# Performance work log

Hardware: AMD Instinct MI355X
Metric: run time of the kernel (lower is better)

Reference implementation:

```python
import jax, jax.numpy as jnp
import numpy as np

B, S, H, W, T, D = 256, 128, 14, 14, 12, 512


def _lin(key, fan_in, fan_out):
    k1, k2 = jax.random.split(key)
    bound = 1.0 / np.sqrt(fan_in)
    Wm = jax.random.uniform(k1, (fan_in, fan_out), jnp.float32, -bound, bound)
    b = jax.random.uniform(k2, (fan_out,), jnp.float32, -bound, bound)
    return Wm, b


def setup_inputs() -> dict:
    key = jax.random.key(0)
    ks = jax.random.split(key, 20)
    inp = {
        "ci_1": jax.random.normal(ks[0], (B, D), jnp.float32),
        "mi_1": jax.random.normal(ks[1], (B, D), jnp.float32),
        "q": jax.random.normal(ks[2], (B, D), jnp.float32),
        "cws": jax.random.normal(ks[3], (B, S, D), jnp.float32),
        "K": jax.random.normal(ks[4], (B, H, W, D), jnp.float32),
        "C_past": jax.random.normal(ks[5], (B, T, D), jnp.float32),
        "M_past": jax.random.normal(ks[6], (B, T, D), jnp.float32),
    }
    inp["W_cq"], inp["b_cq"] = _lin(ks[7], D, D)          # control_qi
    inp["W_cqi"], inp["b_cqi"] = _lin(ks[8], 2 * D, D)    # cqi_linear
    inp["W_cai"], inp["b_cai"] = _lin(ks[9], D, 1)        # cais_linear
    inp["W_rm"], inp["b_rm"] = _lin(ks[10], D, D)         # memory_read_m
    inp["W_rk"], inp["b_rk"] = _lin(ks[11], D, D)         # memory_read_k
    inp["W_rik"], inp["b_rik"] = _lin(ks[12], 2 * D, D)   # memory_read_ik
    inp["W_rci"], inp["b_rci"] = _lin(ks[13], D, D)       # memory_read_ci_i
    inp["W_wrm"], inp["b_wrm"] = _lin(ks[14], 2 * D, D)   # memory_write_ri_mi_1
    inp["W_wcc"], inp["b_wcc"] = _lin(ks[15], D, 1)       # memory_write_ci_cj
    inp["W_wsa"], inp["b_wsa"] = _lin(ks[16], D, D)       # memory_write_mi_sa
    inp["W_winfo"], inp["b_winfo"] = _lin(ks[17], D, D)   # memory_write_mi_info
    inp["W_wci"], inp["b_wci"] = _lin(ks[18], D, 1)       # memory_write_ci
    return inp


def reference(ci_1, mi_1, q, cws, K, C_past, M_past,
              W_cq, b_cq, W_cqi, b_cqi, W_cai, b_cai,
              W_rm, b_rm, W_rk, b_rk, W_rik, b_rik, W_rci, b_rci,
              W_wrm, b_wrm, W_wcc, b_wcc, W_wsa, b_wsa,
              W_winfo, b_winfo, W_wci, b_wci):
    # ---- control ----
    qi = q @ W_cq + b_cq                                        # [B,D]
    cqi = jnp.concatenate([ci_1, qi], axis=1) @ W_cqi + b_cqi   # [B,D]
    cqi_cws = cqi[:, None, :] * cws                             # [B,S,D]
    cai = cqi_cws @ W_cai + b_cai                               # [B,S,1]
    cvis = jax.nn.softmax(cai, axis=1)
    ci = (cvis * cws).sum(axis=1)                               # [B,D]

    # ---- read ----
    Ii = (mi_1 @ W_rm + b_rm)[:, None, None, :] * (K @ W_rk + b_rk)  # [B,H,W,D]
    Ii_prime = jnp.concatenate([Ii, K], axis=3) @ W_rik + b_rik      # [B,H,W,D]
    rai = (ci[:, None, None, :] * Ii_prime) @ W_rci + b_rci          # [B,H,W,D]
    rvi = jax.nn.softmax(rai, axis=1)   # softmax over H
    rvi = jax.nn.softmax(rvi, axis=2)   # then softmax of those probs over W (faithful)
    ri = (rvi * K).sum(axis=(1, 2))                                  # [B,D]

    # ---- write ----
    mi_info = jnp.concatenate([ri, mi_1], axis=1) @ W_wrm + b_wrm    # [B,D]
    ci_cj = ci[:, None, :] * C_past                                  # [B,T,D]
    saij = jax.nn.softmax(ci_cj @ W_wcc + b_wcc, axis=1)             # [B,T,1]
    mi_sa = (saij * M_past).sum(axis=1)                              # [B,D]
    mi_prime = (mi_sa @ W_wsa + b_wsa) + (mi_info @ W_winfo + b_winfo)
    gate = jax.nn.sigmoid(ci @ W_wci + b_wci)                        # [B,1]
    mi = gate * mi_1 + (1.0 - gate) * mi_prime
    return (ci, mi)
```

## Files before the change

kernel.cpp:

```cpp
#include <hip/hip_runtime.h>
#include <hip/hip_bf16.h>

typedef unsigned short u16;
typedef __attribute__((ext_vector_type(8))) short short8;
typedef __attribute__((ext_vector_type(4))) float f4;

static __device__ __forceinline__ float b2f(u16 u) {
    union { unsigned int i; float f; } x; x.i = ((unsigned int)u) << 16; return x.f;
}
static __device__ __forceinline__ u16 f2b(float f) {
    union { float f; unsigned int i; } x; x.f = f;
    unsigned int r = x.i + 0x7fffu + ((x.i >> 16) & 1u);
    return (u16)(r >> 16);
}
static __device__ __forceinline__ float wave_reduce_sum(float v) {
    #pragma unroll
    for (int off = 32; off > 0; off >>= 1) v += __shfl_down(v, off, 64);
    return v;
}
static __device__ __forceinline__ void gl2lds(const void* g, void* l) {
    __builtin_amdgcn_global_load_lds(
        (const __attribute__((address_space(1))) void*)g,
        (__attribute__((address_space(3))) void*)l, 16, 0, 0);
}

__global__ __launch_bounds__(256) void conv_f32_bf16(
    const float* __restrict__ src, u16* __restrict__ dst, int n)
{
    int i = (blockIdx.x * 256 + threadIdx.x) * 4;
    if (i >= n) return;
    float4 v = *(const float4*)(src + i);
    union { u16 u[4]; uint2 d; } o;
    o.u[0] = f2b(v.x); o.u[1] = f2b(v.y); o.u[2] = f2b(v.z); o.u[3] = f2b(v.w);
    *(uint2*)(dst + i) = o.d;
}

__global__ __launch_bounds__(256) void transpose_k(
    const float* __restrict__ in, u16* __restrict__ out,
    int K, int N, int out_stride, int k_off)
{
    __shared__ float t[32][33];
    int kb = blockIdx.x * 32, nb = blockIdx.y * 32;
    int tx = threadIdx.x, ty = threadIdx.y;
    #pragma unroll
    for (int i = 0; i < 4; i++)
        t[ty + i * 8][tx] = in[(size_t)(kb + ty + i * 8) * N + nb + tx];
    __syncthreads();
    #pragma unroll
    for (int i = 0; i < 4; i++)
        out[(size_t)(nb + ty + i * 8) * out_stride + k_off + kb + tx] =
            f2b(t[tx][ty + i * 8]);
}

template<int MT, int NT>
__global__ __launch_bounds__(256) void gemm_mfma(
    const u16* __restrict__ A0, const u16* __restrict__ A1,
    int M, int K0, int K1, int N,
    const u16* __restrict__ Bt,
    const float* __restrict__ bias0, const float* __restrict__ bias1,
    int epi_mode, const float* __restrict__ E, int m_div,
    const float* __restrict__ gate, const float* __restrict__ mi1,
    void* __restrict__ Cout, int out_f32)
{
    constexpr int BM = MT * 32, BN = NT * 32;
    constexpr int STG = (BM + BN) * 32;
    constexpr int NPF = MT / 2 + NT / 2;
    constexpr int STAGE_B = 3 * STG * 2;
    __shared__ __align__(16) char smem[STAGE_B];
    short* stg = (short*)smem;

    int tid  = threadIdx.x;
    int wave = tid >> 6, lane = tid & 63;
    int wm = wave >> 1, wn = wave & 1;
    int lrow = lane & 15, quad = lane >> 4;

    int gx = gridDim.x, gy = gridDim.y;
    int bx = blockIdx.x, by = blockIdx.y;
    if ((gy & 7) == 0) {
        int lin = by * gx + bx;
        int xcd = lin & 7, j = lin >> 3;
        by = xcd * (gy >> 3) + j / gx;
        bx = j % gx;
    }
    int bm0 = by * BM, bn0 = bx * BN;
    int Ktot = K0 + K1;
    int KT = Ktot >> 5;

    int r16 = lane >> 2, cc = lane & 3;
    int sw = (r16 >> 1) & 3;
    int coff = (cc ^ sw) * 8;

    auto stage = [&](int s, int k0) {
        const u16* asrc; int lda;
        if (k0 < K0) { asrc = A0 + k0; lda = K0; }
        else         { asrc = A1 + (k0 - K0); lda = K1; }
        short* As = stg + s * STG;
        short* Bs = As + BM * 32;
        #pragma unroll
        for (int i = 0; i < MT / 2; i++) {
            int ar = wave * (BM / 4) + 16 * i;
            gl2lds(asrc + (size_t)(bm0 + ar + r16) * lda + coff, As + ar * 32);
        }
        #pragma unroll
        for (int i = 0; i < NT / 2; i++) {
            int br = wave * (BN / 4) + 16 * i;
            gl2lds(Bt + (size_t)(bn0 + br + r16) * Ktot + k0 + coff, Bs + br * 32);
        }
    };

    f4 acc[MT][NT];
    #pragma unroll
    for (int i = 0; i < MT; i++)
        #pragma unroll
        for (int j = 0; j < NT; j++)
            acc[i][j] = (f4){0.f, 0.f, 0.f, 0.f};

    stage(0, 0);
    if (KT > 1) stage(1, 32);
    int sb = 0;
    int sw2 = (lrow >> 1) & 3;
    for (int kt = 0; kt < KT; kt++) {
        if (kt + 1 < KT) {
            if constexpr (NPF == 2)
                asm volatile("s_waitcnt vmcnt(2) lgkmcnt(0)\ns_barrier" ::: "memory");
            else
                asm volatile("s_waitcnt vmcnt(0) lgkmcnt(0)\ns_barrier" ::: "memory");
        } else {
            asm volatile("s_waitcnt vmcnt(0) lgkmcnt(0)\ns_barrier" ::: "memory");
        }
        const short* Ab = stg + sb * STG;
        const short* Bb = Ab + BM * 32;
        if (kt + 2 < KT) {
            int s2 = sb + 2; if (s2 >= 3) s2 -= 3;
            stage(s2, (kt + 2) * 32);
        }
        short8 af[MT], bfr[NT];
        #pragma unroll
        for (int mt = 0; mt < MT; mt++)
            af[mt] = *(const short8*)&Ab[(wm * (MT * 16) + mt * 16 + lrow) * 32 + (quad ^ sw2) * 8];
        #pragma unroll
        for (int nt = 0; nt < NT; nt++)
            bfr[nt] = *(const short8*)&Bb[(wn * (NT * 16) + nt * 16 + lrow) * 32 + (quad ^ sw2) * 8];
        #pragma unroll
        for (int mt = 0; mt < MT; mt++)
            #pragma unroll
            for (int nt = 0; nt < NT; nt++)
                acc[mt][nt] = __builtin_amdgcn_mfma_f32_16x16x32_bf16(
                    af[mt], bfr[nt], acc[mt][nt], 0, 0, 0);
        sb = (sb + 1 == 3) ? 0 : sb + 1;
    }

    #pragma unroll
    for (int nt = 0; nt < NT; nt++) {
        int n = bn0 + wn * (NT * 16) + nt * 16 + lrow;
        float bv = 0.f;
        if (bias0) bv += bias0[n];
        if (bias1) bv += bias1[n];
        #pragma unroll
        for (int mt = 0; mt < MT; mt++) {
            #pragma unroll
            for (int r = 0; r < 4; r++) {
                int m = bm0 + wm * (MT * 16) + mt * 16 + quad * 4 + r;
                float v = acc[mt][nt][r] + bv;
                if (epi_mode == 1) {
                    v *= E[(size_t)(m / m_div) * N + n];
                } else if (epi_mode == 2) {
                    float g = gate[m];
                    v = g * mi1[(size_t)m * N + n] + (1.f - g) * v;
                }
                if (out_f32) ((float*)Cout)[(size_t)m * N + n] = v;
                else         ((u16*)Cout)[(size_t)m * N + n] = f2b(v);
            }
        }
    }
}

__global__ __launch_bounds__(512, 2) void fused_read(
    const u16* __restrict__ kbf, int M,
    const u16* __restrict__ Wrk,  const float* __restrict__ brk,  const float* __restrict__ E1,
    const u16* __restrict__ Wrik, const float* __restrict__ brik, const float* __restrict__ E2,
    const u16* __restrict__ Wrci, const float* __restrict__ brci,
    u16* __restrict__ rai)
{
    __shared__ __align__(16) char smem[139264];
    short* g_tile = (short*)smem;
    short* stgbase = (short*)(smem + 65536);

    int tid = threadIdx.x, wave = tid >> 6, lane = tid & 63;
    int wr = wave >> 2, wc = wave & 3;
    int lrow = lane & 15, quad = lane >> 4;
    int r16 = lane >> 2, cc = lane & 3;
    int sw = (r16 >> 1) & 3;
    int coff = (cc ^ sw) * 8;
    int sw2 = (lrow >> 1) & 3;

    int bid = blockIdx.x;
    { int nb = gridDim.x; if ((nb & 7) == 0) { int x = bid & 7, j = bid >> 3; bid = x * (nb >> 3) + j; } }
    int bm0 = bid * 64;

    auto stageB = [&](short* bf, const u16* Wt, int ldk, int k0) {
        short* Bs = bf + 2048;
        #pragma unroll
        for (int i = 0; i < 4; i++) {
            int br = wave * 64 + i * 16;
            gl2lds(Wt + (size_t)(br + r16) * ldk + k0 + coff, Bs + br * 32);
        }
    };
    auto stageA = [&](short* bf, int k0) {
        if (wave < 4) {
            int ar = wave * 16;
            gl2lds(kbf + (size_t)(bm0 + ar + r16) * 512 + k0 + coff, bf + ar * 32);
        }
    };

    f4 acc[2][8];
    auto clr = [&]() {
        #pragma unroll
        for (int t = 0; t < 2; t++)
            #pragma unroll
            for (int nt = 0; nt < 8; nt++)
                acc[t][nt] = (f4){0.f, 0.f, 0.f, 0.f};
    };

    auto kstep = [&](const short* bf, int aMode, int kc0) {
        short8 af[2], bfrag[8];
        #pragma unroll
        for (int t = 0; t < 2; t++) {
            int R = wr * 32 + t * 16 + lrow;
            if (aMode == 0)
                af[t] = *(const short8*)&bf[R * 32 + (quad ^ sw2) * 8];
            else {
                int kc = kc0 + quad;
                af[t] = *(const short8*)&g_tile[R * 512 + ((kc ^ (R & 7)) << 3)];
            }
        }
        const short* Bs = bf + 2048;
        #pragma unroll
        for (int nt = 0; nt < 8; nt++)
            bfrag[nt] = *(const short8*)&Bs[(wc * 128 + nt * 16 + lrow) * 32 + (quad ^ sw2) * 8];
        #pragma unroll
        for (int t = 0; t < 2; t++)
            #pragma unroll
            for (int nt = 0; nt < 8; nt++)
                acc[t][nt] = __builtin_amdgcn_mfma_f32_16x16x32_bf16(
                    af[t], bfrag[nt], acc[t][nt], 0, 0, 0);
    };

    int b0 = bm0 / 196, b1 = (bm0 + 63) / 196;
    int rsw = (b1 != b0) ? (b1 * 196 - bm0) : 64;
    auto epi_to_gtile = [&](const float* bias, const float* E) {
        #pragma unroll
        for (int nt = 0; nt < 8; nt++) {
            int n = wc * 128 + nt * 16 + lrow;
            float bv = bias[n];
            float e0 = E[(size_t)b0 * 512 + n];
            float e1 = E[(size_t)b1 * 512 + n];
            #pragma unroll
            for (int t = 0; t < 2; t++)
                #pragma unroll
                for (int r = 0; r < 4; r++) {
                    int row = wr * 32 + t * 16 + quad * 4 + r;
                    float e = (row < rsw) ? e0 : e1;
                    u16 h = f2b((acc[t][nt][r] + bv) * e);
                    int chunk = (n >> 3) ^ (row & 7);
                    g_tile[row * 512 + chunk * 8 + (n & 7)] = (short)h;
                }
        }
    };

    clr();
    stageA(stgbase, 0); stageB(stgbase, Wrk, 512, 0);
    for (int kt = 0; kt < 16; kt++) {
        short* cur = stgbase + (kt & 1) * 18432;
        short* nxt = stgbase + ((kt & 1) ^ 1) * 18432;
        if (kt + 1 < 16) {
            stageA(nxt, (kt + 1) * 32); stageB(nxt, Wrk, 512, (kt + 1) * 32);
            if (wave < 4) asm volatile("s_waitcnt vmcnt(5) lgkmcnt(0)\ns_barrier" ::: "memory");
            else          asm volatile("s_waitcnt vmcnt(4) lgkmcnt(0)\ns_barrier" ::: "memory");
        } else
            asm volatile("s_waitcnt vmcnt(0) lgkmcnt(0)\ns_barrier" ::: "memory");
        kstep(cur, 0, 0);
        __syncthreads();
    }
    epi_to_gtile(brk, E1);
    __syncthreads();

    clr();
    stageB(stgbase, Wrik, 1024, 0);
    for (int kt = 0; kt < 16; kt++) {
        short* cur = stgbase + (kt & 1) * 18432;
        short* nxt = stgbase + ((kt & 1) ^ 1) * 18432;
        if (kt + 1 < 16) {
            stageB(nxt, Wrik, 1024, (kt + 1) * 32);
            asm volatile("s_waitcnt vmcnt(4) lgkmcnt(0)\ns_barrier" ::: "memory");
        } else
            asm volatile("s_waitcnt vmcnt(0) lgkmcnt(0)\ns_barrier" ::: "memory");
        kstep(cur, 1, kt * 4);
        __syncthreads();
    }
    stageA(stgbase, 0); stageB(stgbase, Wrik, 1024, 512);
    for (int kt = 0; kt < 16; kt++) {
        short* cur = stgbase + (kt & 1) * 18432;
        short* nxt = stgbase + ((kt & 1) ^ 1) * 18432;
        if (kt + 1 < 16) {
            stageA(nxt, (kt + 1) * 32); stageB(nxt, Wrik, 1024, 512 + (kt + 1) * 32);
            if (wave < 4) asm volatile("s_waitcnt vmcnt(5) lgkmcnt(0)\ns_barrier" ::: "memory");
            else          asm volatile("s_waitcnt vmcnt(4) lgkmcnt(0)\ns_barrier" ::: "memory");
        } else
            asm volatile("s_waitcnt vmcnt(0) lgkmcnt(0)\ns_barrier" ::: "memory");
        kstep(cur, 0, 0);
        __syncthreads();
    }
    epi_to_gtile(brik, E2);
    __syncthreads();

    clr();
    stageB(stgbase, Wrci, 512, 0);
    for (int kt = 0; kt < 16; kt++) {
        short* cur = stgbase + (kt & 1) * 18432;
        short* nxt = stgbase + ((kt & 1) ^ 1) * 18432;
        if (kt + 1 < 16) {
            stageB(nxt, Wrci, 512, (kt + 1) * 32);
            asm volatile("s_waitcnt vmcnt(4) lgkmcnt(0)\ns_barrier" ::: "memory");
        } else
            asm volatile("s_waitcnt vmcnt(0) lgkmcnt(0)\ns_barrier" ::: "memory");
        kstep(cur, 1, kt * 4);
        __syncthreads();
    }
    #pragma unroll
    for (int nt = 0; nt < 8; nt++) {
        int n = wc * 128 + nt * 16 + lrow;
        float bv = brci[n];
        #pragma unroll
        for (int t = 0; t < 2; t++)
            #pragma unroll
            for (int r = 0; r < 4; r++) {
                int row = wr * 32 + t * 16 + quad * 4 + r;
                g_tile[row * 512 + n] = (short)f2b(acc[t][nt][r] + bv);
            }
    }
    __syncthreads();
    #pragma unroll
    for (int p = 0; p < 8; p++) {
        int idx = p * 512 + tid;
        short8 v = *(const short8*)&g_tile[idx * 8];
        *(short8*)&rai[(size_t)bm0 * 512 + (size_t)idx * 8] = v;
    }
}

__global__ __launch_bounds__(256) void control_attn(
    const float* __restrict__ cqi, const float* __restrict__ cws,
    const float* __restrict__ Wcai, const float* __restrict__ bcai,
    float* __restrict__ ci_f32, float* __restrict__ ci_out)
{
    int b = blockIdx.x, tid = threadIdx.x;
    __shared__ float tW[512];
    __shared__ float p[128];
    __shared__ float inv_l;
    for (int d = tid; d < 512; d += 256)
        tW[d] = cqi[(size_t)b * 512 + d] * Wcai[d];
    __syncthreads();
    int wave = tid >> 6, lane = tid & 63;
    const float* cwsb = cws + (size_t)b * 128 * 512;
    for (int s = wave; s < 128; s += 4) {
        const float* row = cwsb + (size_t)s * 512 + lane * 8;
        float acc = 0.f;
        #pragma unroll
        for (int j = 0; j < 8; j++) acc += tW[lane * 8 + j] * row[j];
        acc = wave_reduce_sum(acc);
        if (lane == 0) p[s] = acc + bcai[0];
    }
    __syncthreads();
    if (tid == 0) {
        float m = -1e30f;
        for (int s = 0; s < 128; s++) m = fmaxf(m, p[s]);
        float l = 0.f;
        for (int s = 0; s < 128; s++) { float e = __expf(p[s] - m); p[s] = e; l += e; }
        inv_l = 1.f / l;
    }
    __syncthreads();
    float inv = inv_l;
    for (int d = tid; d < 512; d += 256) {
        float acc = 0.f;
        for (int s = 0; s < 128; s++) acc += p[s] * cwsb[(size_t)s * 512 + d];
        acc *= inv;
        ci_f32[(size_t)b * 512 + d] = acc;
        ci_out[(size_t)b * 512 + d] = acc;
    }
}

__global__ __launch_bounds__(256) void read_reduce(
    const u16* __restrict__ rai, const u16* __restrict__ Kb, u16* __restrict__ ri)
{
    int b = blockIdx.x >> 1;
    int d = ((blockIdx.x & 1) << 8) + threadIdx.x;
    const u16* rb = rai + (size_t)b * 196 * 512 + d;
    const u16* kb = Kb + (size_t)b * 196 * 512 + d;
    float m1[14], il1[14];
    #pragma unroll
    for (int w = 0; w < 14; w++) {
        float m = -1e30f, s = 0.f;
        #pragma unroll
        for (int h = 0; h < 14; h++) {
            float v = b2f(rb[(size_t)(h * 14 + w) * 512]);
            float nm = fmaxf(m, v);
            s = s * __expf(m - nm) + __expf(v - nm);
            m = nm;
        }
        m1[w] = m; il1[w] = 1.f / s;
    }
    float acc = 0.f;
    #pragma unroll
    for (int h = 0; h < 14; h++) {
        float pv[14], ss = 0.f;
        #pragma unroll
        for (int w = 0; w < 14; w++) {
            float pr = __expf(b2f(rb[(size_t)(h * 14 + w) * 512]) - m1[w]) * il1[w];
            float e = __expf(pr);
            pv[w] = e; ss += e;
        }
        float il2 = 1.f / ss;
        #pragma unroll
        for (int w = 0; w < 14; w++)
            acc += pv[w] * il2 * b2f(kb[(size_t)(h * 14 + w) * 512]);
    }
    ri[(size_t)b * 512 + d] = f2b(acc);
}

__global__ __launch_bounds__(256) void write_attn(
    const float* __restrict__ ci_f32, const float* __restrict__ C_past,
    const float* __restrict__ M_past,
    const float* __restrict__ Wwcc, const float* __restrict__ bwcc,
    const float* __restrict__ Wwci, const float* __restrict__ bwci,
    u16* __restrict__ mi_sa, float* __restrict__ gate)
{
    int b = blockIdx.x, tid = threadIdx.x;
    __shared__ float c[512];
    __shared__ float pt[12];
    __shared__ float red[256];
    for (int d = tid; d < 512; d += 256) c[d] = ci_f32[(size_t)b * 512 + d];
    __syncthreads();
    float g = 0.f;
    for (int d = tid; d < 512; d += 256) g += c[d] * Wwci[d];
    red[tid] = g;
    __syncthreads();
    for (int s = 128; s > 0; s >>= 1) {
        if (tid < s) red[tid] += red[tid + s];
        __syncthreads();
    }
    int wave = tid >> 6, lane = tid & 63;
    const float* cp = C_past + (size_t)b * 12 * 512;
    for (int t = wave; t < 12; t += 4) {
        float acc = 0.f;
        #pragma unroll
        for (int j = 0; j < 8; j++) {
            int d = lane * 8 + j;
            acc += c[d] * Wwcc[d] * cp[(size_t)t * 512 + d];
        }
        acc = wave_reduce_sum(acc);
        if (lane == 0) pt[t] = acc + bwcc[0];
    }
    __syncthreads();
    if (tid == 0) {
        float m = -1e30f;
        for (int t = 0; t < 12; t++) m = fmaxf(m, pt[t]);
        float l = 0.f;
        for (int t = 0; t < 12; t++) { float e = __expf(pt[t] - m); pt[t] = e; l += e; }
        float invl = 1.f / l;
        for (int t = 0; t < 12; t++) pt[t] *= invl;
        gate[b] = 1.f / (1.f + __expf(-(red[0] + bwci[0])));
    }
    __syncthreads();
    const float* mp = M_past + (size_t)b * 12 * 512;
    for (int d = tid; d < 512; d += 256) {
        float acc = 0.f;
        #pragma unroll
        for (int t = 0; t < 12; t++) acc += pt[t] * mp[(size_t)t * 512 + d];
        mi_sa[(size_t)b * 512 + d] = f2b(acc);
    }
}

extern "C" void kernel_launch(void* const* d_in, const int* in_sizes, int n_in,
                              void* d_out, int out_size, void* d_ws, size_t ws_size,
                              hipStream_t stream) {
    (void)in_sizes; (void)n_in; (void)out_size;
    const int B = 256, D = 512, HW = 196;

    const float* ci_1   = (const float*)d_in[0];
    const float* mi_1   = (const float*)d_in[1];
    const float* q      = (const float*)d_in[2];
    const float* cws    = (const float*)d_in[3];
    const float* Kin    = (const float*)d_in[4];
    const float* C_past = (const float*)d_in[5];
    const float* M_past = (const float*)d_in[6];
    const float* W_cq   = (const float*)d_in[7];
    const float* b_cq   = (const float*)d_in[8];
    const float* W_cqi  = (const float*)d_in[9];
    const float* b_cqi  = (const float*)d_in[10];
    const float* W_cai  = (const float*)d_in[11];
    const float* b_cai  = (const float*)d_in[12];
    const float* W_rm   = (const float*)d_in[13];
    const float* b_rm   = (const float*)d_in[14];
    const float* W_rk   = (const float*)d_in[15];
    const float* b_rk   = (const float*)d_in[16];
    const float* W_rik  = (const float*)d_in[17];
    const float* b_rik  = (const float*)d_in[18];
    const float* W_rci  = (const float*)d_in[19];
    const float* b_rci  = (const float*)d_in[20];
    const float* W_wrm  = (const float*)d_in[21];
    const float* b_wrm  = (const float*)d_in[22];
    const float* W_wcc  = (const float*)d_in[23];
    const float* b_wcc  = (const float*)d_in[24];
    const float* W_wsa  = (const float*)d_in[25];
    const float* b_wsa  = (const float*)d_in[26];
    const float* W_winfo= (const float*)d_in[27];
    const float* b_winfo= (const float*)d_in[28];
    const float* W_wci  = (const float*)d_in[29];
    const float* b_wci  = (const float*)d_in[30];

    float* out_ci = (float*)d_out;
    float* out_mi = (float*)d_out + (size_t)B * D;

    char* ws = (char*)d_ws;
    size_t off = 0;
    auto alloc = [&](size_t bytes) -> void* {
        void* p = ws + off; off += (bytes + 255) & ~(size_t)255; return p;
    };
    u16* wt_cq    = (u16*)alloc((size_t)D * D * 2);
    u16* wt_cqi   = (u16*)alloc((size_t)D * 2 * D * 2);
    u16* wt_rm    = (u16*)alloc((size_t)D * D * 2);
    u16* wt_rk    = (u16*)alloc((size_t)D * D * 2);
    u16* wt_rik   = (u16*)alloc((size_t)D * 2 * D * 2);
    u16* wt_rci   = (u16*)alloc((size_t)D * D * 2);
    u16* wt_wrm   = (u16*)alloc((size_t)D * 2 * D * 2);
    u16* wt_wsi   = (u16*)alloc((size_t)D * 2 * D * 2);
    u16* qb       = (u16*)alloc((size_t)B * D * 2);
    u16* cib      = (u16*)alloc((size_t)B * D * 2);
    u16* mib      = (u16*)alloc((size_t)B * D * 2);
    u16* qi_buf   = (u16*)alloc((size_t)B * D * 2);
    float* cqi_f32= (float*)alloc((size_t)B * D * 4);
    float* rm_f32 = (float*)alloc((size_t)B * D * 4);
    float* ci_f32 = (float*)alloc((size_t)B * D * 4);
    u16* ri_buf   = (u16*)alloc((size_t)B * D * 2);
    u16* misa_buf = (u16*)alloc((size_t)B * D * 2);
    u16* minfo_buf= (u16*)alloc((size_t)B * D * 2);
    float* gate_b = (float*)alloc((size_t)B * 4);

    int chunk_b = 256;
    while (chunk_b > 32) {
        size_t need = off + 2 * (((size_t)chunk_b * HW * D * 2 + 255) & ~(size_t)255);
        if (need <= ws_size) break;
        chunk_b >>= 1;
    }
    u16* kbf  = (u16*)alloc((size_t)chunk_b * HW * D * 2);
    u16* big1 = (u16*)alloc((size_t)chunk_b * HW * D * 2);

    dim3 tb(32, 8);
    transpose_k<<<dim3(D / 32, D / 32), tb, 0, stream>>>(W_cq,   wt_cq,  D,     D, D,     0);
    transpose_k<<<dim3(2 * D / 32, D / 32), tb, 0, stream>>>(W_cqi, wt_cqi, 2 * D, D, 2 * D, 0);
    transpose_k<<<dim3(D / 32, D / 32), tb, 0, stream>>>(W_rm,   wt_rm,  D,     D, D,     0);
    transpose_k<<<dim3(D / 32, D / 32), tb, 0, stream>>>(W_rk,   wt_rk,  D,     D, D,     0);
    transpose_k<<<dim3(2 * D / 32, D / 32), tb, 0, stream>>>(W_rik, wt_rik, 2 * D, D, 2 * D, 0);
    transpose_k<<<dim3(D / 32, D / 32), tb, 0, stream>>>(W_rci,  wt_rci, D,     D, D,     0);
    transpose_k<<<dim3(2 * D / 32, D / 32), tb, 0, stream>>>(W_wrm, wt_wrm, 2 * D, D, 2 * D, 0);
    transpose_k<<<dim3(D / 32, D / 32), tb, 0, stream>>>(W_wsa,  wt_wsi, D,     D, 2 * D, 0);
    transpose_k<<<dim3(D / 32, D / 32), tb, 0, stream>>>(W_winfo,wt_wsi, D,     D, 2 * D, D);

    int nbd = B * D;
    conv_f32_bf16<<<nbd / 1024, 256, 0, stream>>>(q, qb, nbd);
    conv_f32_bf16<<<nbd / 1024, 256, 0, stream>>>(ci_1, cib, nbd);
    conv_f32_bf16<<<nbd / 1024, 256, 0, stream>>>(mi_1, mib, nbd);

    dim3 gsmall(D / 64, B / 64);

    gemm_mfma<2,2><<<gsmall, 256, 0, stream>>>(qb, nullptr, B, D, 0, D, wt_cq, b_cq, nullptr,
                                               0, nullptr, 1, nullptr, nullptr, qi_buf, 0);
    gemm_mfma<2,2><<<gsmall, 256, 0, stream>>>(cib, qi_buf, B, D, D, D, wt_cqi, b_cqi, nullptr,
                                               0, nullptr, 1, nullptr, nullptr, cqi_f32, 1);
    control_attn<<<B, 256, 0, stream>>>(cqi_f32, cws, W_cai, b_cai, ci_f32, out_ci);
    gemm_mfma<2,2><<<gsmall, 256, 0, stream>>>(mib, nullptr, B, D, 0, D, wt_rm, b_rm, nullptr,
                                               0, nullptr, 1, nullptr, nullptr, rm_f32, 1);

    for (int c = 0; c < B; c += chunk_b) {
        int mrows = chunk_b * HW;
        const float* Kc = Kin + (size_t)c * HW * D;
        conv_f32_bf16<<<(mrows * D) / 1024, 256, 0, stream>>>(Kc, kbf, mrows * D);
        fused_read<<<mrows / 64, 512, 0, stream>>>(
            kbf, mrows,
            wt_rk,  b_rk,  rm_f32 + (size_t)c * D,
            wt_rik, b_rik, ci_f32 + (size_t)c * D,
            wt_rci, b_rci,
            big1);
        read_reduce<<<chunk_b * 2, 256, 0, stream>>>(big1, kbf, ri_buf + (size_t)c * D);
    }

    gemm_mfma<2,2><<<gsmall, 256, 0, stream>>>(ri_buf, mib, B, D, D, D, wt_wrm, b_wrm, nullptr,
                                               0, nullptr, 1, nullptr, nullptr, minfo_buf, 0);
    write_attn<<<B, 256, 0, stream>>>(ci_f32, C_past, M_past, W_wcc, b_wcc, W_wci, b_wci,
                                      misa_buf, gate_b);
    gemm_mfma<2,2><<<gsmall, 256, 0, stream>>>(misa_buf, minfo_buf, B, D, D, D, wt_wsi,
                                               b_wsa, b_winfo, 2, nullptr, 1, gate_b, mi_1,
                                               out_mi, 1);
}
```

Before: 634.6 us.

## Load weight fragments directly into registers instead of staging through LDS

The fused read kernel stops staging the weight (B) tiles in shared memory. Each wave now loads its B fragments from global memory straight into registers, double-buffered across k-steps, and only the A tile still goes through LDS. This shrinks shared memory from about 136KB to 72KB, which may allow more blocks per CU and removes the LDS writes and reads for B. In exchange it adds register pressure, makes global loads less coalesced and duplicated across the waves sharing a column, and relies on hand-written vmcnt counts that must match the new number of loads.

Result: slower. 911.1 us (+43.6%).

```diff
diff --git a/kernel.cpp b/kernel.cpp
--- a/kernel.cpp
+++ b/kernel.cpp
@@ -182,9 +182,10 @@
     const u16* __restrict__ Wrci, const float* __restrict__ brci,
     u16* __restrict__ rai)
 {
-    __shared__ __align__(16) char smem[139264];
+    __shared__ __align__(16) char smem[73728];
     short* g_tile = (short*)smem;
-    short* stgbase = (short*)(smem + 65536);
+    short* stg0 = (short*)(smem + 65536);
+    short* stg1 = stg0 + 2048;
 
     int tid = threadIdx.x, wave = tid >> 6, lane = tid & 63;
     int wr = wave >> 2, wc = wave & 3;
@@ -198,14 +199,6 @@
     { int nb = gridDim.x; if ((nb & 7) == 0) { int x = bid & 7, j = bid >> 3; bid = x * (nb >> 3) + j; } }
     int bm0 = bid * 64;
 
-    auto stageB = [&](short* bf, const u16* Wt, int ldk, int k0) {
-        short* Bs = bf + 2048;
-        #pragma unroll
-        for (int i = 0; i < 4; i++) {
-            int br = wave * 64 + i * 16;
-            gl2lds(Wt + (size_t)(br + r16) * ldk + k0 + coff, Bs + br * 32);
-        }
-    };
     auto stageA = [&](short* bf, int k0) {
         if (wave < 4) {
             int ar = wave * 16;
@@ -222,28 +215,58 @@
                 acc[t][nt] = (f4){0.f, 0.f, 0.f, 0.f};
     };
 
-    auto kstep = [&](const short* bf, int aMode, int kc0) {
-        short8 af[2], bfrag[8];
+    short8 bfA[8], bfB[8];
+
+    auto loadB = [&](short8 (&dst)[8], const u16* W, int ldk, int k0) {
+        #pragma unroll
+        for (int nt = 0; nt < 8; nt++)
+            dst[nt] = *(const short8*)&W[(size_t)(wc * 128 + nt * 16 + lrow) * ldk + k0 + quad * 8];
+    };
+
+    auto kstepA = [&](const short* Abuf, const short8 (&bf)[8]) {
+        short8 af[2];
         #pragma unroll
         for (int t = 0; t < 2; t++) {
             int R = wr * 32 + t * 16 + lrow;
-            if (aMode == 0)
-                af[t] = *(const short8*)&bf[R * 32 + (quad ^ sw2) * 8];
-            else {
-                int kc = kc0 + quad;
-                af[t] = *(const short8*)&g_tile[R * 512 + ((kc ^ (R & 7)) << 3)];
-            }
-        }
-        const short* Bs = bf + 2048;
-        #pragma unroll
-        for (int nt = 0; nt < 8; nt++)
-            bfrag[nt] = *(const short8*)&Bs[(wc * 128 + nt * 16 + lrow) * 32 + (quad ^ sw2) * 8];
+            af[t] = *(const short8*)&Abuf[R * 32 + (quad ^ sw2) * 8];
+        }
         #pragma unroll
         for (int t = 0; t < 2; t++)
             #pragma unroll
             for (int nt = 0; nt < 8; nt++)
                 acc[t][nt] = __builtin_amdgcn_mfma_f32_16x16x32_bf16(
-                    af[t], bfrag[nt], acc[t][nt], 0, 0, 0);
+                    af[t], bf[nt], acc[t][nt], 0, 0, 0);
+    };
+
+    auto kstepG = [&](const short8 (&bf)[8], int kc0) {
+        short8 af[2];
+        #pragma unroll
+        for (int t = 0; t < 2; t++) {
+            int R = wr * 32 + t * 16 + lrow;
+            int kc = kc0 + quad;
+            af[t] = *(const short8*)&g_tile[R * 512 + ((kc ^ (R & 7)) << 3)];
+        }
+        #pragma unroll
+        for (int t = 0; t < 2; t++)
+            #pragma unroll
+            for (int nt = 0; nt < 8; nt++)
+                acc[t][nt] = __builtin_amdgcn_mfma_f32_16x16x32_bf16(
+                    af[t], bf[nt], acc[t][nt], 0, 0, 0);
+    };
+
+    auto stagedStep = [&](int kt, short* curA, short* nxtA,
+                          short8 (&bcur)[8], short8 (&bnxt)[8],
+                          const u16* W, int ldk, int kbase) {
+        if (kt + 1 < 16) {
+            stageA(nxtA, kbase + (kt + 1) * 32);
+            loadB(bnxt, W, ldk, kbase + (kt + 1) * 32);
+            if (wave < 4) asm volatile("s_waitcnt vmcnt(9)\ns_barrier" ::: "memory");
+            else          asm volatile("s_barrier" ::: "memory");
+        } else {
+            asm volatile("s_waitcnt vmcnt(0) lgkmcnt(0)\ns_barrier" ::: "memory");
+        }
+        kstepA(curA, bcur);
+        asm volatile("s_waitcnt lgkmcnt(0)\ns_barrier" ::: "memory");
     };
 
     int b0 = bm0 / 196, b1 = (bm0 + 63) / 196;
@@ -269,64 +292,42 @@
     };
 
     clr();
-    stageA(stgbase, 0); stageB(stgbase, Wrk, 512, 0);
-    for (int kt = 0; kt < 16; kt++) {
-        short* cur = stgbase + (kt & 1) * 18432;
-        short* nxt = stgbase + ((kt & 1) ^ 1) * 18432;
-        if (kt + 1 < 16) {
-            stageA(nxt, (kt + 1) * 32); stageB(nxt, Wrk, 512, (kt + 1) * 32);
-            if (wave < 4) asm volatile("s_waitcnt vmcnt(5) lgkmcnt(0)\ns_barrier" ::: "memory");
-            else          asm volatile("s_waitcnt vmcnt(4) lgkmcnt(0)\ns_barrier" ::: "memory");
-        } else
-            asm volatile("s_waitcnt vmcnt(0) lgkmcnt(0)\ns_barrier" ::: "memory");
-        kstep(cur, 0, 0);
-        __syncthreads();
+    stageA(stg0, 0);
+    loadB(bfA, Wrk, 512, 0);
+    for (int kt = 0; kt < 16; kt += 2) {
+        stagedStep(kt,     stg0, stg1, bfA, bfB, Wrk, 512, 0);
+        stagedStep(kt + 1, stg1, stg0, bfB, bfA, Wrk, 512, 0);
     }
     epi_to_gtile(brk, E1);
     __syncthreads();
 
     clr();
-    stageB(stgbase, Wrik, 1024, 0);
-    for (int kt = 0; kt < 16; kt++) {
-        short* cur = stgbase + (kt & 1) * 18432;
-        short* nxt = stgbase + ((kt & 1) ^ 1) * 18432;
-        if (kt + 1 < 16) {
-            stageB(nxt, Wrik, 1024, (kt + 1) * 32);
-            asm volatile("s_waitcnt vmcnt(4) lgkmcnt(0)\ns_barrier" ::: "memory");
-        } else
-            asm volatile("s_waitcnt vmcnt(0) lgkmcnt(0)\ns_barrier" ::: "memory");
-        kstep(cur, 1, kt * 4);
-        __syncthreads();
-    }
-    stageA(stgbase, 0); stageB(stgbase, Wrik, 1024, 512);
-    for (int kt = 0; kt < 16; kt++) {
-        short* cur = stgbase + (kt & 1) * 18432;
-        short* nxt = stgbase + ((kt & 1) ^ 1) * 18432;
-        if (kt + 1 < 16) {
-            stageA(nxt, (kt + 1) * 32); stageB(nxt, Wrik, 1024, 512 + (kt + 1) * 32);
-            if (wave < 4) asm volatile("s_waitcnt vmcnt(5) lgkmcnt(0)\ns_barrier" ::: "memory");
-            else          asm volatile("s_waitcnt vmcnt(4) lgkmcnt(0)\ns_barrier" ::: "memory");
-        } else
-            asm volatile("s_waitcnt vmcnt(0) lgkmcnt(0)\ns_barrier" ::: "memory");
-        kstep(cur, 0, 0);
-        __syncthreads();
+    loadB(bfA, Wrik, 1024, 0);
+    for (int kt = 0; kt < 16; kt += 2) {
+        loadB(bfB, Wrik, 1024, (kt + 1) * 32);
+        kstepG(bfA, kt * 4);
+        if (kt + 2 < 16) loadB(bfA, Wrik, 1024, (kt + 2) * 32);
+        kstepG(bfB, (kt + 1) * 4);
+    }
+    __syncthreads();
+    stageA(stg0, 0);
+    loadB(bfA, Wrik, 1024, 512);
+    for (int kt = 0; kt < 16; kt += 2) {
+        stagedStep(kt,     stg0, stg1, bfA, bfB, Wrik, 1024, 512);
+        stagedStep(kt + 1, stg1, stg0, bfB, bfA, Wrik, 1024, 512);
     }
     epi_to_gtile(brik, E2);
     __syncthreads();
 
     clr();
-    stageB(stgbase, Wrci, 512, 0);
-    for (int kt = 0; kt < 16; kt++) {
-        short* cur = stgbase + (kt & 1) * 18432;
-        short* nxt = stgbase + ((kt & 1) ^ 1) * 18432;
-        if (kt + 1 < 16) {
-            stageB(nxt, Wrci, 512, (kt + 1) * 32);
-            asm volatile("s_waitcnt vmcnt(4) lgkmcnt(0)\ns_barrier" ::: "memory");
-        } else
-            asm volatile("s_waitcnt vmcnt(0) lgkmcnt(0)\ns_barrier" ::: "memory");
-        kstep(cur, 1, kt * 4);
-        __syncthreads();
-    }
+    loadB(bfA, Wrci, 512, 0);
+    for (int kt = 0; kt < 16; kt += 2) {
+        loadB(bfB, Wrci, 512, (kt + 1) * 32);
+        kstepG(bfA, kt * 4);
+        if (kt + 2 < 16) loadB(bfA, Wrci, 512, (kt + 2) * 32);
+        kstepG(bfB, (kt + 1) * 4);
+    }
+    __syncthreads();
     #pragma unroll
     for (int nt = 0; nt < 8; nt++) {
         int n = wc * 128 + nt * 16 + lrow;
```
